# Optimization experiments

Hardware: AMD Instinct MI355X
Metric: run time of the kernel (lower is better)

## Reference

```python
import jax, jax.numpy as jnp
import numpy as np

I = 512  # input_size
H = 512  # hidden_size
B = 16384  # batch


def setup_inputs() -> dict:
    key = jax.random.key(0)
    ks = jax.random.split(key, 8)
    s_g = 1.0 / np.sqrt(I + H)
    s_i = 1.0 / np.sqrt(I)
    s_h = 1.0 / np.sqrt(H)
    return {
        "input": jax.random.normal(ks[0], (B, I), dtype=jnp.float32),
        "hidden": jax.random.normal(ks[1], (B, H), dtype=jnp.float32),
        "W_gate": jax.random.uniform(ks[2], (2 * H, I + H), minval=-s_g, maxval=s_g, dtype=jnp.float32),
        "b_gate": jax.random.uniform(ks[3], (2 * H,), minval=-s_g, maxval=s_g, dtype=jnp.float32),
        "W_i": jax.random.uniform(ks[4], (H, I), minval=-s_i, maxval=s_i, dtype=jnp.float32),
        "b_i": jax.random.uniform(ks[5], (H,), minval=-s_i, maxval=s_i, dtype=jnp.float32),
        "W_h": jax.random.uniform(ks[6], (H, H), minval=-s_h, maxval=s_h, dtype=jnp.float32),
        "b_h": jax.random.uniform(ks[7], (H,), minval=-s_h, maxval=s_h, dtype=jnp.float32),
    }


def reference(input, hidden, W_gate, b_gate, W_i, b_i, W_h, b_h):
    # combined linear for r/z gates: [B, I+H] @ [I+H, 2H]
    combined = jnp.concatenate([input, hidden], axis=1)
    gates = combined @ W_gate.T + b_gate  # [B, 2H]
    r_gate = jax.nn.sigmoid(gates[:, :H])
    z_gate = jax.nn.sigmoid(gates[:, H:])
    i_gate = input @ W_i.T + b_i   # [B, H]
    h_gate = hidden @ W_h.T + b_h  # [B, H]
    n_gate = jnp.tanh(i_gate + r_gate * h_gate)
    new_hidden = (1.0 - z_gate) * n_gate + z_gate * hidden
    return new_hidden  # dropout p=0.0 -> identity
```

## Files before the change

### kernel.cpp

```cpp
#include <hip/hip_runtime.h>
#include <cstdint>
#include <cstddef>


typedef __attribute__((ext_vector_type(8))) __bf16 bf16x8;
typedef __attribute__((ext_vector_type(4))) float f32x4;
typedef __attribute__((ext_vector_type(8))) unsigned short u16x8;

__device__ __forceinline__ unsigned short f2bf(float f) {
    unsigned u = __builtin_bit_cast(unsigned, f);
    return (unsigned short)((u + 0x7fffu + ((u >> 16) & 1u)) >> 16);
}

__global__ void prep_x(const float* __restrict__ inp, const float* __restrict__ hid,
                       unsigned short* __restrict__ X) {
    int t = blockIdx.x * 256 + threadIdx.x;
    int b = t >> 7;
    int j = (t & 127) << 3;
    const float* src = (j < 512) ? (inp + (size_t)b * 512 + j)
                                 : (hid + (size_t)b * 512 + (j - 512));
    u16x8 o;
#pragma unroll
    for (int e = 0; e < 8; ++e) o[e] = f2bf(src[e]);
    *reinterpret_cast<u16x8*>(X + (size_t)b * 1024 + j) = o;
}

__global__ void prep_w(const float* __restrict__ Wg, const float* __restrict__ Wi,
                       const float* __restrict__ Wh,
                       unsigned short* __restrict__ Wrz, unsigned short* __restrict__ Wih) {
    int t = blockIdx.x * 256 + threadIdx.x;
    if (t < 131072) {
        const float* src = Wg + (size_t)t * 8;
        u16x8 o;
#pragma unroll
        for (int e = 0; e < 8; ++e) o[e] = f2bf(src[e]);
        *reinterpret_cast<u16x8*>(Wrz + (size_t)t * 8) = o;
    } else {
        int u = t - 131072;
        int n = u >> 7;
        int k = (u & 127) << 3;
        const float* src = (k < 512) ? (Wi + (size_t)n * 512 + k)
                                     : (Wh + (size_t)n * 512 + (k - 512));
        u16x8 o;
#pragma unroll
        for (int e = 0; e < 8; ++e) o[e] = f2bf(src[e]);
        *reinterpret_cast<u16x8*>(Wih + (size_t)n * 1024 + k) = o;
    }
}

__device__ __forceinline__ void gload16(const void* g, void* l) {
    __builtin_amdgcn_global_load_lds(
        (const __attribute__((address_space(1))) void*)g,
        (__attribute__((address_space(3))) void*)l, 16, 0, 0);
}

__device__ __forceinline__ bf16x8 ldfrag(const unsigned short* base, int row, int ch) {
    const char* p = (const char*)base + row * 128 + ((ch ^ (row & 7)) << 4);
    return *reinterpret_cast<const bf16x8*>(p);
}

__global__ __launch_bounds__(256, 2) void gru_fused(
        const unsigned short* __restrict__ X,
        const unsigned short* __restrict__ Wr,
        const unsigned short* __restrict__ Wz,
        const unsigned short* __restrict__ Wih,
        const float* __restrict__ hidden,
        const float* __restrict__ bgate,
        const float* __restrict__ bi,
        const float* __restrict__ bh,
        float* __restrict__ out) {
    __shared__ unsigned short lX[128 * 64];
    __shared__ unsigned short lR[64 * 64];
    __shared__ unsigned short lZ[64 * 64];
    __shared__ unsigned short lW[64 * 64];

    const int tid = threadIdx.x;
    const int lane = tid & 63;
    const int wid = tid >> 6;
    const int wm = wid >> 1, wn = wid & 1;
    const int bid = blockIdx.x;
    const int bn = bid & 7;
    const int bm = bid >> 3;

    const int rowa = tid >> 3;
    const int lc   = (tid & 7) ^ (rowa & 7);
    const size_t xbase = ((size_t)(bm * 128 + rowa) * 1024 + lc * 8) * 2;
    const size_t wbase = ((size_t)(bn * 64 + rowa) * 1024 + lc * 8) * 2;
    const char* gX = (const char*)X   + xbase;
    const char* gR = (const char*)Wr  + wbase;
    const char* gZ = (const char*)Wz  + wbase;
    const char* gW = (const char*)Wih + wbase;
    char* lXp = (char*)lX + tid * 16;
    char* lRp = (char*)lR + tid * 16;
    char* lZp = (char*)lZ + tid * 16;
    char* lWp = (char*)lW + tid * 16;

    f32x4 accR[4][2], accZ[4][2], accI[4][2], accH[4][2];
#pragma unroll
    for (int i = 0; i < 4; ++i)
#pragma unroll
        for (int j = 0; j < 2; ++j) {
            accR[i][j] = (f32x4){0.f, 0.f, 0.f, 0.f};
            accZ[i][j] = (f32x4){0.f, 0.f, 0.f, 0.f};
            accI[i][j] = (f32x4){0.f, 0.f, 0.f, 0.f};
            accH[i][j] = (f32x4){0.f, 0.f, 0.f, 0.f};
        }

    const int ra = wm * 64 + (lane & 15);
    const int rb = wn * 32 + (lane & 15);
    const int c0 = lane >> 4;

#define MFMA8(ACC, B0, B1)                                                            \
    ACC[0][0] = __builtin_amdgcn_mfma_f32_16x16x32_bf16(a0, B0, ACC[0][0], 0, 0, 0); \
    ACC[1][0] = __builtin_amdgcn_mfma_f32_16x16x32_bf16(a1, B0, ACC[1][0], 0, 0, 0); \
    ACC[2][0] = __builtin_amdgcn_mfma_f32_16x16x32_bf16(a2, B0, ACC[2][0], 0, 0, 0); \
    ACC[3][0] = __builtin_amdgcn_mfma_f32_16x16x32_bf16(a3, B0, ACC[3][0], 0, 0, 0); \
    ACC[0][1] = __builtin_amdgcn_mfma_f32_16x16x32_bf16(a0, B1, ACC[0][1], 0, 0, 0); \
    ACC[1][1] = __builtin_amdgcn_mfma_f32_16x16x32_bf16(a1, B1, ACC[1][1], 0, 0, 0); \
    ACC[2][1] = __builtin_amdgcn_mfma_f32_16x16x32_bf16(a2, B1, ACC[2][1], 0, 0, 0); \
    ACC[3][1] = __builtin_amdgcn_mfma_f32_16x16x32_bf16(a3, B1, ACC[3][1], 0, 0, 0);

#define KSTEP(kt, ACC3)                                                         \
    {                                                                           \
        gload16(gX + (kt) * 128,               lXp);                            \
        gload16(gX + (kt) * 128 +  32 * 2048,  lXp + 4096);                     \
        gload16(gX + (kt) * 128 +  64 * 2048,  lXp + 8192);                     \
        gload16(gX + (kt) * 128 +  96 * 2048,  lXp + 12288);                    \
        gload16(gR + (kt) * 128,               lRp);                            \
        gload16(gR + (kt) * 128 +  32 * 2048,  lRp + 4096);                     \
        gload16(gZ + (kt) * 128,               lZp);                            \
        gload16(gZ + (kt) * 128 +  32 * 2048,  lZp + 4096);                     \
        gload16(gW + (kt) * 128,               lWp);                            \
        gload16(gW + (kt) * 128 +  32 * 2048,  lWp + 4096);                     \
        __syncthreads();                                                        \
        _Pragma("unroll")                                                       \
        for (int ks = 0; ks < 2; ++ks) {                                        \
            const int ch = ks * 4 + c0;                                         \
            bf16x8 a0 = ldfrag(lX, ra,      ch);                                \
            bf16x8 a1 = ldfrag(lX, ra + 16, ch);                                \
            bf16x8 a2 = ldfrag(lX, ra + 32, ch);                                \
            bf16x8 a3 = ldfrag(lX, ra + 48, ch);                                \
            bf16x8 b0 = ldfrag(lR, rb, ch);                                     \
            bf16x8 b1 = ldfrag(lR, rb + 16, ch);                                \
            MFMA8(accR, b0, b1)                                                 \
            b0 = ldfrag(lZ, rb, ch);                                            \
            b1 = ldfrag(lZ, rb + 16, ch);                                       \
            MFMA8(accZ, b0, b1)                                                 \
            b0 = ldfrag(lW, rb, ch);                                            \
            b1 = ldfrag(lW, rb + 16, ch);                                       \
            MFMA8(ACC3, b0, b1)                                                 \
        }                                                                       \
        __syncthreads();                                                        \
    }

    for (int kt = 0; kt < 8; ++kt) KSTEP(kt, accI)
    for (int kt = 8; kt < 16; ++kt) KSTEP(kt, accH)
#undef KSTEP
#undef MFMA8

    const int colb = bn * 64 + wn * 32 + (lane & 15);
    const int rowb = bm * 128 + wm * 64 + ((lane >> 4) << 2);
#pragma unroll
    for (int ni = 0; ni < 2; ++ni) {
        const int n = colb + ni * 16;
        const float bgr = bgate[n];
        const float bgz = bgate[512 + n];
        const float bii = bi[n];
        const float bhh = bh[n];
#pragma unroll
        for (int mi = 0; mi < 4; ++mi) {
#pragma unroll
            for (int r = 0; r < 4; ++r) {
                const int m = rowb + mi * 16 + r;
                const size_t off = (size_t)m * 512 + n;
                float rg = accR[mi][ni][r] + bgr;
                rg = 1.f / (1.f + __expf(-rg));
                float zg = accZ[mi][ni][r] + bgz;
                zg = 1.f / (1.f + __expf(-zg));
                float x = accI[mi][ni][r] + bii + rg * (accH[mi][ni][r] + bhh);
                x = fminf(fmaxf(x, -15.f), 15.f);
                const float e = __expf(2.f * x);
                const float ng = (e - 1.f) / (e + 1.f);
                out[off] = ng + zg * (hidden[off] - ng);
            }
        }
    }
}

extern "C" void kernel_launch(void* const* d_in, const int* in_sizes, int n_in,
                              void* d_out, int out_size, void* d_ws, size_t ws_size,
                              hipStream_t stream) {
    const float* inp = (const float*)d_in[0];
    const float* hid = (const float*)d_in[1];
    const float* Wg  = (const float*)d_in[2];
    const float* bg  = (const float*)d_in[3];
    const float* Wi  = (const float*)d_in[4];
    const float* bi  = (const float*)d_in[5];
    const float* Wh  = (const float*)d_in[6];
    const float* bh  = (const float*)d_in[7];
    float* out = (float*)d_out;

    unsigned short* X   = (unsigned short*)d_ws;
    unsigned short* Wrz = (unsigned short*)((char*)d_ws + 33554432);
    unsigned short* Wih = (unsigned short*)((char*)d_ws + 33554432 + 2097152);

    prep_x<<<8192, 256, 0, stream>>>(inp, hid, X);
    prep_w<<<768, 256, 0, stream>>>(Wg, Wi, Wh, Wrz, Wih);
    gru_fused<<<1024, 256, 0, stream>>>(X, Wrz, Wrz + 512 * 1024, Wih, hid, bg, bi, bh, out);
}
```

Before: 185.0 us.

## Fuse activation bf16 conversion into GEMM and double-buffer weight tiles

After: 222.4 us. 1.2x slower.

```diff
diff --git a/kernel.cpp b/kernel.cpp
--- a/kernel.cpp
+++ b/kernel.cpp
@@ -10,19 +10,6 @@
 __device__ __forceinline__ unsigned short f2bf(float f) {
     unsigned u = __builtin_bit_cast(unsigned, f);
     return (unsigned short)((u + 0x7fffu + ((u >> 16) & 1u)) >> 16);
-}
-
-__global__ void prep_x(const float* __restrict__ inp, const float* __restrict__ hid,
-                       unsigned short* __restrict__ X) {
-    int t = blockIdx.x * 256 + threadIdx.x;
-    int b = t >> 7;
-    int j = (t & 127) << 3;
-    const float* src = (j < 512) ? (inp + (size_t)b * 512 + j)
-                                 : (hid + (size_t)b * 512 + (j - 512));
-    u16x8 o;
-#pragma unroll
-    for (int e = 0; e < 8; ++e) o[e] = f2bf(src[e]);
-    *reinterpret_cast<u16x8*>(X + (size_t)b * 1024 + j) = o;
 }
 
 __global__ void prep_w(const float* __restrict__ Wg, const float* __restrict__ Wi,
@@ -60,19 +47,19 @@
 }
 
 __global__ __launch_bounds__(256, 2) void gru_fused(
-        const unsigned short* __restrict__ X,
+        const float* __restrict__ inp,
+        const float* __restrict__ hid,
         const unsigned short* __restrict__ Wr,
         const unsigned short* __restrict__ Wz,
         const unsigned short* __restrict__ Wih,
-        const float* __restrict__ hidden,
         const float* __restrict__ bgate,
         const float* __restrict__ bi,
         const float* __restrict__ bh,
         float* __restrict__ out) {
     __shared__ unsigned short lX[128 * 64];
-    __shared__ unsigned short lR[64 * 64];
-    __shared__ unsigned short lZ[64 * 64];
-    __shared__ unsigned short lW[64 * 64];
+    __shared__ unsigned short lR[2][64 * 64];
+    __shared__ unsigned short lZ[2][64 * 64];
+    __shared__ unsigned short lW[2][64 * 64];
 
     const int tid = threadIdx.x;
     const int lane = tid & 63;
@@ -83,17 +70,18 @@
     const int bm = bid >> 3;
 
     const int rowa = tid >> 3;
-    const int lc   = (tid & 7) ^ (rowa & 7);
-    const size_t xbase = ((size_t)(bm * 128 + rowa) * 1024 + lc * 8) * 2;
+    const int lc = (tid & 7) ^ (rowa & 7);
     const size_t wbase = ((size_t)(bn * 64 + rowa) * 1024 + lc * 8) * 2;
-    const char* gX = (const char*)X   + xbase;
-    const char* gR = (const char*)Wr  + wbase;
-    const char* gZ = (const char*)Wz  + wbase;
-    const char* gW = (const char*)Wih + wbase;
-    char* lXp = (char*)lX + tid * 16;
-    char* lRp = (char*)lR + tid * 16;
-    char* lZp = (char*)lZ + tid * 16;
-    char* lWp = (char*)lW + tid * 16;
+    const char* gR0 = (const char*)Wr + wbase;  const char* gR1 = gR0 + 65536;
+    const char* gZ0 = (const char*)Wz + wbase;  const char* gZ1 = gZ0 + 65536;
+    const char* gW0 = (const char*)Wih + wbase; const char* gW1 = gW0 + 65536;
+
+    const int xr = tid >> 1;
+    const int xc = (tid & 1) * 32;
+    const float* xsi = inp + (size_t)(bm * 128 + xr) * 512 + xc;
+    const float* xsh = hid + (size_t)(bm * 128 + xr) * 512 + xc;
+
+    float xv[32];
 
     f32x4 accR[4][2], accZ[4][2], accI[4][2], accH[4][2];
 #pragma unroll
@@ -109,6 +97,24 @@
     const int ra = wm * 64 + (lane & 15);
     const int rb = wn * 32 + (lane & 15);
     const int c0 = lane >> 4;
+
+#define XLOAD(t) { const float* s_ = ((t) < 8 ? xsi : xsh) + ((t) & 7) * 64;          \
+    _Pragma("unroll") for (int j_ = 0; j_ < 8; ++j_)                                  \
+        *reinterpret_cast<f32x4*>(xv + j_ * 4) = reinterpret_cast<const f32x4*>(s_)[j_]; }
+
+#define WLOAD(t, b) {                                                    \
+    gload16(gR0 + (t) * 128, (char*)lR[b] + tid * 16);                   \
+    gload16(gR1 + (t) * 128, (char*)lR[b] + tid * 16 + 4096);            \
+    gload16(gZ0 + (t) * 128, (char*)lZ[b] + tid * 16);                   \
+    gload16(gZ1 + (t) * 128, (char*)lZ[b] + tid * 16 + 4096);            \
+    gload16(gW0 + (t) * 128, (char*)lW[b] + tid * 16);                   \
+    gload16(gW1 + (t) * 128, (char*)lW[b] + tid * 16 + 4096); }
+
+#define XWRITE() {                                                                     \
+    _Pragma("unroll") for (int j2 = 0; j2 < 4; ++j2) {                                 \
+        u16x8 w_;                                                                      \
+        _Pragma("unroll") for (int e_ = 0; e_ < 8; ++e_) w_[e_] = f2bf(xv[j2 * 8 + e_]); \
+        *reinterpret_cast<u16x8*>(lX + xr * 64 + ((((xc >> 3) + j2) ^ (xr & 7)) << 3)) = w_; } }
 
 #define MFMA8(ACC, B0, B1)                                                            \
     ACC[0][0] = __builtin_amdgcn_mfma_f32_16x16x32_bf16(a0, B0, ACC[0][0], 0, 0, 0); \
@@ -120,43 +126,47 @@
     ACC[2][1] = __builtin_amdgcn_mfma_f32_16x16x32_bf16(a2, B1, ACC[2][1], 0, 0, 0); \
     ACC[3][1] = __builtin_amdgcn_mfma_f32_16x16x32_bf16(a3, B1, ACC[3][1], 0, 0, 0);
 
-#define KSTEP(kt, ACC3)                                                         \
-    {                                                                           \
-        gload16(gX + (kt) * 128,               lXp);                            \
-        gload16(gX + (kt) * 128 +  32 * 2048,  lXp + 4096);                     \
-        gload16(gX + (kt) * 128 +  64 * 2048,  lXp + 8192);                     \
-        gload16(gX + (kt) * 128 +  96 * 2048,  lXp + 12288);                    \
-        gload16(gR + (kt) * 128,               lRp);                            \
-        gload16(gR + (kt) * 128 +  32 * 2048,  lRp + 4096);                     \
-        gload16(gZ + (kt) * 128,               lZp);                            \
-        gload16(gZ + (kt) * 128 +  32 * 2048,  lZp + 4096);                     \
-        gload16(gW + (kt) * 128,               lWp);                            \
-        gload16(gW + (kt) * 128 +  32 * 2048,  lWp + 4096);                     \
-        __syncthreads();                                                        \
-        _Pragma("unroll")                                                       \
-        for (int ks = 0; ks < 2; ++ks) {                                        \
-            const int ch = ks * 4 + c0;                                         \
-            bf16x8 a0 = ldfrag(lX, ra,      ch);                                \
-            bf16x8 a1 = ldfrag(lX, ra + 16, ch);                                \
-            bf16x8 a2 = ldfrag(lX, ra + 32, ch);                                \
-            bf16x8 a3 = ldfrag(lX, ra + 48, ch);                                \
-            bf16x8 b0 = ldfrag(lR, rb, ch);                                     \
-            bf16x8 b1 = ldfrag(lR, rb + 16, ch);                                \
-            MFMA8(accR, b0, b1)                                                 \
-            b0 = ldfrag(lZ, rb, ch);                                            \
-            b1 = ldfrag(lZ, rb + 16, ch);                                       \
-            MFMA8(accZ, b0, b1)                                                 \
-            b0 = ldfrag(lW, rb, ch);                                            \
-            b1 = ldfrag(lW, rb + 16, ch);                                       \
-            MFMA8(ACC3, b0, b1)                                                 \
-        }                                                                       \
-        __syncthreads();                                                        \
-    }
-
-    for (int kt = 0; kt < 8; ++kt) KSTEP(kt, accI)
-    for (int kt = 8; kt < 16; ++kt) KSTEP(kt, accH)
-#undef KSTEP
+#define COMPUTE(b, ACC3)                                                 \
+    _Pragma("unroll") for (int ks = 0; ks < 2; ++ks) {                   \
+        const int ch = ks * 4 + c0;                                      \
+        bf16x8 a0 = ldfrag(lX, ra, ch);                                  \
+        bf16x8 a1 = ldfrag(lX, ra + 16, ch);                             \
+        bf16x8 a2 = ldfrag(lX, ra + 32, ch);                             \
+        bf16x8 a3 = ldfrag(lX, ra + 48, ch);                             \
+        bf16x8 b0 = ldfrag(lR[b], rb, ch);                               \
+        bf16x8 b1 = ldfrag(lR[b], rb + 16, ch);                          \
+        MFMA8(accR, b0, b1)                                              \
+        b0 = ldfrag(lZ[b], rb, ch);                                      \
+        b1 = ldfrag(lZ[b], rb + 16, ch);                                 \
+        MFMA8(accZ, b0, b1)                                              \
+        b0 = ldfrag(lW[b], rb, ch);                                      \
+        b1 = ldfrag(lW[b], rb + 16, ch);                                 \
+        MFMA8(ACC3, b0, b1)                                              \
+    }
+
+    XLOAD(0)
+    WLOAD(0, 0)
+    XWRITE()
+    asm volatile("s_waitcnt vmcnt(0) lgkmcnt(0)" ::: "memory");
+    __builtin_amdgcn_s_barrier();
+
+#pragma unroll
+    for (int t = 0; t < 15; ++t) {
+        const int nb = (t + 1) & 1;
+        XLOAD(t + 1)
+        WLOAD(t + 1, nb)
+        if (t < 8) { COMPUTE(t & 1, accI) } else { COMPUTE(t & 1, accH) }
+        __builtin_amdgcn_s_barrier();
+        XWRITE()
+        asm volatile("s_waitcnt vmcnt(0) lgkmcnt(0)" ::: "memory");
+        __builtin_amdgcn_s_barrier();
+    }
+    COMPUTE(1, accH)
+#undef COMPUTE
 #undef MFMA8
+#undef XWRITE
+#undef WLOAD
+#undef XLOAD
 
     const int colb = bn * 64 + wn * 32 + (lane & 15);
     const int rowb = bm * 128 + wm * 64 + ((lane >> 4) << 2);
@@ -181,7 +191,7 @@
                 x = fminf(fmaxf(x, -15.f), 15.f);
                 const float e = __expf(2.f * x);
                 const float ng = (e - 1.f) / (e + 1.f);
-                out[off] = ng + zg * (hidden[off] - ng);
+                out[off] = ng + zg * (hid[off] - ng);
             }
         }
     }
@@ -200,11 +210,10 @@
     const float* bh  = (const float*)d_in[7];
     float* out = (float*)d_out;
 
-    unsigned short* X   = (unsigned short*)d_ws;
-    unsigned short* Wrz = (unsigned short*)((char*)d_ws + 33554432);
-    unsigned short* Wih = (unsigned short*)((char*)d_ws + 33554432 + 2097152);
-
-    prep_x<<<8192, 256, 0, stream>>>(inp, hid, X);
+    unsigned short* Wrz = (unsigned short*)d_ws;
+    unsigned short* Wih = (unsigned short*)((char*)d_ws + 2097152);
+
     prep_w<<<768, 256, 0, stream>>>(Wg, Wi, Wh, Wrz, Wih);
-    gru_fused<<<1024, 256, 0, stream>>>(X, Wrz, Wrz + 512 * 1024, Wih, hid, bg, bi, bh, out);
-}
+    gru_fused<<<1024, 256, 0, stream>>>(inp, hid, Wrz, Wrz + 512 * 1024, Wih,
+                                        bg, bi, bh, out);
+}
```

## Double-buffer LDS tiles with K=32 stages and raise occupancy target

Applied to the files above, without the earlier changes.

Result: slower. 313.5 us (+69.5%).

```diff
diff --git a/kernel.cpp b/kernel.cpp
--- a/kernel.cpp
+++ b/kernel.cpp
@@ -54,25 +54,22 @@
         (__attribute__((address_space(3))) void*)l, 16, 0, 0);
 }
 
-__device__ __forceinline__ bf16x8 ldfrag(const unsigned short* base, int row, int ch) {
-    const char* p = (const char*)base + row * 128 + ((ch ^ (row & 7)) << 4);
+__device__ __forceinline__ bf16x8 ldfrag32(const unsigned short* base, int row, int c0) {
+    const char* p = (const char*)base + row * 64 + ((c0 ^ ((row >> 1) & 3)) << 4);
     return *reinterpret_cast<const bf16x8*>(p);
 }
 
-__global__ __launch_bounds__(256, 2) void gru_fused(
+__global__ __launch_bounds__(256, 4) void gru_fused(
         const unsigned short* __restrict__ X,
         const unsigned short* __restrict__ Wr,
         const unsigned short* __restrict__ Wz,
         const unsigned short* __restrict__ Wih,
-        const float* __restrict__ hidden,
+        const float* __restrict__ hid,
         const float* __restrict__ bgate,
         const float* __restrict__ bi,
         const float* __restrict__ bh,
         float* __restrict__ out) {
-    __shared__ unsigned short lX[128 * 64];
-    __shared__ unsigned short lR[64 * 64];
-    __shared__ unsigned short lZ[64 * 64];
-    __shared__ unsigned short lW[64 * 64];
+    __shared__ unsigned short lds[2][10240];
 
     const int tid = threadIdx.x;
     const int lane = tid & 63;
@@ -82,18 +79,13 @@
     const int bn = bid & 7;
     const int bm = bid >> 3;
 
-    const int rowa = tid >> 3;
-    const int lc   = (tid & 7) ^ (rowa & 7);
-    const size_t xbase = ((size_t)(bm * 128 + rowa) * 1024 + lc * 8) * 2;
-    const size_t wbase = ((size_t)(bn * 64 + rowa) * 1024 + lc * 8) * 2;
-    const char* gX = (const char*)X   + xbase;
-    const char* gR = (const char*)Wr  + wbase;
-    const char* gZ = (const char*)Wz  + wbase;
-    const char* gW = (const char*)Wih + wbase;
-    char* lXp = (char*)lX + tid * 16;
-    char* lRp = (char*)lR + tid * 16;
-    char* lZp = (char*)lZ + tid * 16;
-    char* lWp = (char*)lW + tid * 16;
+    const int srow = tid >> 2;
+    const int lc = (tid & 3) ^ ((tid >> 3) & 3);
+    const char* gX0 = (const char*)X   + ((size_t)(bm * 128 + srow) * 1024 + lc * 8) * 2;
+    const char* gX1 = gX0 + 64 * 2048;
+    const char* gR  = (const char*)Wr  + ((size_t)(bn * 64 + srow) * 1024 + lc * 8) * 2;
+    const char* gZ  = (const char*)Wz  + ((size_t)(bn * 64 + srow) * 1024 + lc * 8) * 2;
+    const char* gW  = (const char*)Wih + ((size_t)(bn * 64 + srow) * 1024 + lc * 8) * 2;
 
     f32x4 accR[4][2], accZ[4][2], accI[4][2], accH[4][2];
 #pragma unroll
@@ -109,6 +101,13 @@
     const int ra = wm * 64 + (lane & 15);
     const int rb = wn * 32 + (lane & 15);
     const int c0 = lane >> 4;
+
+#define STAGE(t, b) {                                                  \
+        gload16(gX0 + (t) * 64, (char*)lds[b] + tid * 16);             \
+        gload16(gX1 + (t) * 64, (char*)lds[b] + 4096 + tid * 16);      \
+        gload16(gR  + (t) * 64, (char*)lds[b] + 8192 + tid * 16);      \
+        gload16(gZ  + (t) * 64, (char*)lds[b] + 12288 + tid * 16);     \
+        gload16(gW  + (t) * 64, (char*)lds[b] + 16384 + tid * 16); }
 
 #define MFMA8(ACC, B0, B1)                                                            \
     ACC[0][0] = __builtin_amdgcn_mfma_f32_16x16x32_bf16(a0, B0, ACC[0][0], 0, 0, 0); \
@@ -120,43 +119,40 @@
     ACC[2][1] = __builtin_amdgcn_mfma_f32_16x16x32_bf16(a2, B1, ACC[2][1], 0, 0, 0); \
     ACC[3][1] = __builtin_amdgcn_mfma_f32_16x16x32_bf16(a3, B1, ACC[3][1], 0, 0, 0);
 
-#define KSTEP(kt, ACC3)                                                         \
-    {                                                                           \
-        gload16(gX + (kt) * 128,               lXp);                            \
-        gload16(gX + (kt) * 128 +  32 * 2048,  lXp + 4096);                     \
-        gload16(gX + (kt) * 128 +  64 * 2048,  lXp + 8192);                     \
-        gload16(gX + (kt) * 128 +  96 * 2048,  lXp + 12288);                    \
-        gload16(gR + (kt) * 128,               lRp);                            \
-        gload16(gR + (kt) * 128 +  32 * 2048,  lRp + 4096);                     \
-        gload16(gZ + (kt) * 128,               lZp);                            \
-        gload16(gZ + (kt) * 128 +  32 * 2048,  lZp + 4096);                     \
-        gload16(gW + (kt) * 128,               lWp);                            \
-        gload16(gW + (kt) * 128 +  32 * 2048,  lWp + 4096);                     \
-        __syncthreads();                                                        \
-        _Pragma("unroll")                                                       \
-        for (int ks = 0; ks < 2; ++ks) {                                        \
-            const int ch = ks * 4 + c0;                                         \
-            bf16x8 a0 = ldfrag(lX, ra,      ch);                                \
-            bf16x8 a1 = ldfrag(lX, ra + 16, ch);                                \
-            bf16x8 a2 = ldfrag(lX, ra + 32, ch);                                \
-            bf16x8 a3 = ldfrag(lX, ra + 48, ch);                                \
-            bf16x8 b0 = ldfrag(lR, rb, ch);                                     \
-            bf16x8 b1 = ldfrag(lR, rb + 16, ch);                                \
-            MFMA8(accR, b0, b1)                                                 \
-            b0 = ldfrag(lZ, rb, ch);                                            \
-            b1 = ldfrag(lZ, rb + 16, ch);                                       \
-            MFMA8(accZ, b0, b1)                                                 \
-            b0 = ldfrag(lW, rb, ch);                                            \
-            b1 = ldfrag(lW, rb + 16, ch);                                       \
-            MFMA8(ACC3, b0, b1)                                                 \
-        }                                                                       \
-        __syncthreads();                                                        \
-    }
-
-    for (int kt = 0; kt < 8; ++kt) KSTEP(kt, accI)
-    for (int kt = 8; kt < 16; ++kt) KSTEP(kt, accH)
-#undef KSTEP
+#define COMPUTE(b, ACC3) {                                             \
+        const unsigned short* bp = lds[b];                             \
+        bf16x8 a0 = ldfrag32(bp, ra,      c0);                         \
+        bf16x8 a1 = ldfrag32(bp, ra + 16, c0);                         \
+        bf16x8 a2 = ldfrag32(bp, ra + 32, c0);                         \
+        bf16x8 a3 = ldfrag32(bp, ra + 48, c0);                         \
+        bf16x8 b0 = ldfrag32(bp + 4096, rb, c0);                       \
+        bf16x8 b1 = ldfrag32(bp + 4096, rb + 16, c0);                  \
+        MFMA8(accR, b0, b1)                                            \
+        b0 = ldfrag32(bp + 6144, rb, c0);                              \
+        b1 = ldfrag32(bp + 6144, rb + 16, c0);                         \
+        MFMA8(accZ, b0, b1)                                            \
+        b0 = ldfrag32(bp + 8192, rb, c0);                              \
+        b1 = ldfrag32(bp + 8192, rb + 16, c0);                         \
+        MFMA8(ACC3, b0, b1) }
+
+    STAGE(0, 0)
+    __syncthreads();
+
+#pragma unroll 2
+    for (int t = 0; t < 16; ++t) {
+        STAGE(t + 1, (t + 1) & 1)
+        COMPUTE(t & 1, accI)
+        __syncthreads();
+    }
+#pragma unroll 2
+    for (int t = 16; t < 32; ++t) {
+        if (t < 31) STAGE(t + 1, (t + 1) & 1)
+        COMPUTE(t & 1, accH)
+        __syncthreads();
+    }
+#undef COMPUTE
 #undef MFMA8
+#undef STAGE
 
     const int colb = bn * 64 + wn * 32 + (lane & 15);
     const int rowb = bm * 128 + wm * 64 + ((lane >> 4) << 2);
@@ -181,7 +177,7 @@
                 x = fminf(fmaxf(x, -15.f), 15.f);
                 const float e = __expf(2.f * x);
                 const float ng = (e - 1.f) / (e + 1.f);
-                out[off] = ng + zg * (hidden[off] - ng);
+                out[off] = ng + zg * (hid[off] - ng);
             }
         }
     }
@@ -206,5 +202,6 @@
 
     prep_x<<<8192, 256, 0, stream>>>(inp, hid, X);
     prep_w<<<768, 256, 0, stream>>>(Wg, Wi, Wh, Wrz, Wih);
-    gru_fused<<<1024, 256, 0, stream>>>(X, Wrz, Wrz + 512 * 1024, Wih, hid, bg, bi, bh, out);
-}
+    gru_fused<<<1024, 256, 0, stream>>>(X, Wrz, Wrz + 512 * 1024, Wih,
+                                        hid, bg, bi, bh, out);
+}
```
